# Performance work log

Hardware: AMD Instinct MI355X
Metric: run time of the kernel (lower is better)

## Reference

```python
import jax, jax.numpy as jnp
import numpy as np


def gru_layer(x, w_ih, w_hh, b_ih, b_hh):
    """PyTorch-semantics single GRU layer, batch_first.
    x: [B, T, in], w_ih: [3H, in], w_hh: [3H, H], gate order (r, z, n).
    Returns [B, T, H]. Initial hidden state is zeros.
    """
    H = w_hh.shape[1]
    # Precompute input-side gate projections for all timesteps (one big GEMM).
    xg = jnp.einsum('bti,gi->btg', x, w_ih) + b_ih  # [B, T, 3H]

    def step(h, xg_t):
        hg = h @ w_hh.T + b_hh                      # [B, 3H]
        xr, xz, xn = jnp.split(xg_t, 3, axis=-1)
        hr, hz, hn = jnp.split(hg, 3, axis=-1)
        r = jax.nn.sigmoid(xr + hr)
        z = jax.nn.sigmoid(xz + hz)
        n = jnp.tanh(xn + r * hn)
        h_new = (1.0 - z) * n + z * h
        return h_new, h_new

    h0 = jnp.zeros((x.shape[0], H), dtype=x.dtype)
    _, ys = jax.lax.scan(step, h0, jnp.swapaxes(xg, 0, 1))  # scan over T
    return jnp.swapaxes(ys, 0, 1)                           # [B, T, H]


def _make_layer(key, in_dim, hidden):
    k = 1.0 / np.sqrt(hidden)
    k1, k2, k3, k4 = jax.random.split(key, 4)
    w_ih = jax.random.uniform(k1, (3 * hidden, in_dim), jnp.float32, -k, k)
    w_hh = jax.random.uniform(k2, (3 * hidden, hidden), jnp.float32, -k, k)
    b_ih = jax.random.uniform(k3, (3 * hidden,), jnp.float32, -k, k)
    b_hh = jax.random.uniform(k4, (3 * hidden,), jnp.float32, -k, k)
    return w_ih, w_hh, b_ih, b_hh


def setup_inputs() -> dict:
    key = jax.random.key(0)
    B, C0, T = 32, 256, 2048
    H1, H2 = 512, 1024  # block0: 256->512 (2 layers), block1: 512->1024 (2 layers)
    keys = jax.random.split(key, 5)
    inp = {"x": jax.random.normal(keys[0], (B, C0, T), dtype=jnp.float32)}
    layer_dims = [(C0, H1), (H1, H1), (H1, H2), (H2, H2)]
    names = ['00', '01', '10', '11']
    for nm, (din, h), k in zip(names, layer_dims, keys[1:]):
        w_ih, w_hh, b_ih, b_hh = _make_layer(k, din, h)
        inp[f'w_ih_{nm}'] = w_ih
        inp[f'w_hh_{nm}'] = w_hh
        inp[f'b_ih_{nm}'] = b_ih
        inp[f'b_hh_{nm}'] = b_hh
    return inp


def reference(x,
              w_ih_00, w_hh_00, b_ih_00, b_hh_00,
              w_ih_01, w_hh_01, b_ih_01, b_hh_01,
              w_ih_10, w_hh_10, b_ih_10, b_hh_10,
              w_ih_11, w_hh_11, b_ih_11, b_hh_11):
    h = jnp.transpose(x, (0, 2, 1))  # [B, T, C]
    # Block 0 (2 stacked layers)
    h = gru_layer(h, w_ih_00, w_hh_00, b_ih_00, b_hh_00)
    h = gru_layer(h, w_ih_01, w_hh_01, b_ih_01, b_hh_01)
    # Block 1 (2 stacked layers)
    h = gru_layer(h, w_ih_10, w_hh_10, b_ih_10, b_hh_10)
    h = gru_layer(h, w_ih_11, w_hh_11, b_ih_11, b_hh_11)
    return jnp.transpose(h, (0, 2, 1))  # [B, H_last, T]
```

## Files before the change

### kernel.cpp

```cpp
#include <hip/hip_runtime.h>
#include <cstdint>
#include <cstddef>

typedef __attribute__((ext_vector_type(8))) __bf16 bhalf8;
typedef __attribute__((ext_vector_type(4))) float floatx4;

#define B_ 32
#define T_ 2048
#define CTR_STRIDE 32

__device__ __forceinline__ float sigm_f(float x){ return 1.0f / (1.0f + __expf(-x)); }
__device__ __forceinline__ float tanh_f(float x){ return 1.0f - 2.0f / (1.0f + __expf(2.0f*x)); }

__global__ void k_init(unsigned* bars){
  int i = blockIdx.x * 256 + threadIdx.x;
  if (i < 4 * 8 * CTR_STRIDE) bars[i] = 0u;
}

__global__ void k_cvt(const float* __restrict__ s, __bf16* __restrict__ d, int n){
  int i = blockIdx.x * 256 + threadIdx.x;
  if (i < n) d[i] = (__bf16)s[i];
}

template<typename TI, typename TO>
__global__ void k_transpose(const TI* __restrict__ in, TO* __restrict__ out, int R, int C){
  __shared__ float tile[32][33];
  const size_t bo = (size_t)blockIdx.z * (size_t)R * (size_t)C;
  const int c0 = blockIdx.x * 32, r0 = blockIdx.y * 32;
  const int tx = threadIdx.x, ty = threadIdx.y;
#pragma unroll
  for (int k2 = 0; k2 < 4; ++k2)
    tile[ty + k2*8][tx] = (float)in[bo + (size_t)(r0 + ty + k2*8) * C + c0 + tx];
  __syncthreads();
#pragma unroll
  for (int k2 = 0; k2 < 4; ++k2)
    out[bo + (size_t)(c0 + ty + k2*8) * R + r0 + tx] = (TO)tile[tx][ty + k2*8];
}

__global__ __launch_bounds__(256) void k_gemm(
    const __bf16* __restrict__ A, const __bf16* __restrict__ W,
    const float* __restrict__ bias, __bf16* __restrict__ C,
    int M, int N, int K)
{
  const int tid = threadIdx.x, wave = tid >> 6, lane = tid & 63;
  const int quad = lane >> 4, l = lane & 15;
  const int wy = wave >> 1, wx = wave & 1;
  const size_t rA = (size_t)blockIdx.y * 128 + (size_t)wy * 64;
  const size_t rW = (size_t)blockIdx.x * 128 + (size_t)wx * 64;
  floatx4 acc[4][4] = {};
  for (int k0 = 0; k0 < K; k0 += 32){
    bhalf8 af[4], wf[4];
#pragma unroll
    for (int i = 0; i < 4; ++i)
      af[i] = *(const bhalf8*)(A + (rA + 16*i + l) * (size_t)K + k0 + quad*8);
#pragma unroll
    for (int j = 0; j < 4; ++j)
      wf[j] = *(const bhalf8*)(W + (rW + 16*j + l) * (size_t)K + k0 + quad*8);
#pragma unroll
    for (int i = 0; i < 4; ++i)
#pragma unroll
      for (int j = 0; j < 4; ++j)
        acc[i][j] = __builtin_amdgcn_mfma_f32_16x16x32_bf16(af[i], wf[j], acc[i][j], 0, 0, 0);
  }
#pragma unroll
  for (int j = 0; j < 4; ++j){
    const float bv = bias[rW + 16*j + l];
#pragma unroll
    for (int i = 0; i < 4; ++i)
#pragma unroll
      for (int r = 0; r < 4; ++r)
        C[(rA + 16*i + quad*4 + r) * (size_t)N + rW + 16*j + l] = (__bf16)(acc[i][j][r] + bv);
  }
}

__device__ __forceinline__ void grid_barrier8(unsigned* bars, int my_ctr, unsigned per_target){
  __syncthreads();
  if (threadIdx.x < 8){
    if ((int)threadIdx.x == my_ctr)
      __hip_atomic_fetch_add(bars + my_ctr * CTR_STRIDE, 1u,
                             __ATOMIC_RELAXED, __HIP_MEMORY_SCOPE_AGENT);
    while (__hip_atomic_load(bars + threadIdx.x * CTR_STRIDE,
                             __ATOMIC_RELAXED, __HIP_MEMORY_SCOPE_AGENT) < per_target)
      __builtin_amdgcn_s_sleep(1);
  }
  __syncthreads();
}

__device__ __forceinline__ bhalf8 load_coherent16(const __bf16* p){
  union { unsigned long long q[2]; bhalf8 v; } u;
  u.q[0] = __hip_atomic_load((const unsigned long long*)p,     __ATOMIC_RELAXED, __HIP_MEMORY_SCOPE_AGENT);
  u.q[1] = __hip_atomic_load((const unsigned long long*)p + 1, __ATOMIC_RELAXED, __HIP_MEMORY_SCOPE_AGENT);
  return u.v;
}

template<int H>
__global__ __launch_bounds__(256) void k_scan(
    const __bf16* __restrict__ xg,
    const __bf16* __restrict__ whh,
    const float*  __restrict__ bhh,
    __bf16* __restrict__ hb0, __bf16* __restrict__ hb1,
    __bf16* __restrict__ Y,
    unsigned* __restrict__ bar)
{
  __shared__ float part[2*3*2*16*17];
  __shared__ float hown[32*17];
  const int tid = threadIdx.x, wave = tid >> 6, lane = tid & 63;
  const int quad = lane >> 4, l = lane & 15;
  const int m = wave & 1, kh = wave >> 1;
  const unsigned nblk = gridDim.x;
  const int bid = blockIdx.x;
  const int my_ctr = bid & 7;
  const int swz = (bid & 7) * ((int)nblk >> 3) + (bid >> 3);
  const int u0 = swz * 16;
  const unsigned per_blk = nblk >> 3;

  for (int i = tid; i < 32*16; i += 256){
    int b = i >> 4, u = i & 15;
    hown[b*17 + u] = 0.0f;
  }
  for (int i = tid; i < 32*8; i += 256){
    int b = i >> 3, d = i & 7;
    __hip_atomic_store((unsigned*)(hb0 + (size_t)b*H + u0) + d, 0u,
                       __ATOMIC_RELAXED, __HIP_MEMORY_SCOPE_AGENT);
  }
  const float bh0 = bhh[0*H + u0 + l];
  const float bh1 = bhh[1*H + u0 + l];
  const float bh2 = bhh[2*H + u0 + l];
  const __bf16* wr0 = whh + (size_t)(0*H + u0 + l)*H + kh*(H/2);
  const __bf16* wr1 = whh + (size_t)(1*H + u0 + l)*H + kh*(H/2);
  const __bf16* wr2 = whh + (size_t)(2*H + u0 + l)*H + kh*(H/2);
  const __bf16* ar0 = hb0 + (size_t)(16*m + l)*H + kh*(H/2);
  const __bf16* ar1 = hb1 + (size_t)(16*m + l)*H + kh*(H/2);
  const int b0g = 16*m + quad*4 + 2*kh;

  auto xgi = [&](int b, int t, int g)->size_t {
    return ((size_t)b*T_ + t)*(size_t)(3*H) + (size_t)g*H + u0 + l;
  };

  __bf16 xq[3][2];
#pragma unroll
  for (int g = 0; g < 3; ++g)
#pragma unroll
    for (int r2 = 0; r2 < 2; ++r2)
      xq[g][r2] = xg[xgi(b0g + r2, 0, g)];

  grid_barrier8(bar, my_ctr, per_blk);

  for (int t = 0; t < T_; ++t){
    const __bf16* ar = (t & 1) ? ar1 : ar0;
    __bf16* hd = (t & 1) ? hb0 : hb1;
    floatx4 a0 = {0.f,0.f,0.f,0.f}, a1 = a0, a2 = a0;
#pragma unroll
    for (int ks = 0; ks < H/64; ++ks){
      bhalf8 av = load_coherent16(ar + ks*32 + quad*8);
      bhalf8 w0 = *(const bhalf8*)(wr0 + ks*32 + quad*8);
      bhalf8 w1 = *(const bhalf8*)(wr1 + ks*32 + quad*8);
      bhalf8 w2 = *(const bhalf8*)(wr2 + ks*32 + quad*8);
      a0 = __builtin_amdgcn_mfma_f32_16x16x32_bf16(av, w0, a0, 0, 0, 0);
      a1 = __builtin_amdgcn_mfma_f32_16x16x32_bf16(av, w1, a1, 0, 0, 0);
      a2 = __builtin_amdgcn_mfma_f32_16x16x32_bf16(av, w2, a2, 0, 0, 0);
    }
    const int sb = (kh*6 + m)*272;
#pragma unroll
    for (int r = 0; r < 4; ++r){
      part[sb +        (quad*4+r)*17 + l] = a0[r];
      part[sb + 544  + (quad*4+r)*17 + l] = a1[r];
      part[sb + 1088 + (quad*4+r)*17 + l] = a2[r];
    }
    __syncthreads();
#pragma unroll
    for (int r2 = 0; r2 < 2; ++r2){
      const int row = quad*4 + 2*kh + r2;
      const int bb  = 16*m + row;
      const float hr = part[(0+m)*272 + row*17 + l] + part[(6+m)*272  + row*17 + l] + bh0;
      const float hz = part[(2+m)*272 + row*17 + l] + part[(8+m)*272  + row*17 + l] + bh1;
      const float hn = part[(4+m)*272 + row*17 + l] + part[(10+m)*272 + row*17 + l] + bh2;
      const float xr = (float)xq[0][r2], xz = (float)xq[1][r2], xn = (float)xq[2][r2];
      const float rg = sigm_f(xr + hr);
      const float zg = sigm_f(xz + hz);
      const float ng = tanh_f(xn + rg*hn);
      const float hp = hown[bb*17 + l];
      const float hnew = (1.0f - zg)*ng + zg*hp;
      hown[bb*17 + l] = hnew;
      const __bf16 hb16 = (__bf16)hnew;
      const unsigned mybits = (unsigned)__builtin_bit_cast(unsigned short, hb16);
      const unsigned other  = (unsigned)__shfl_xor((int)mybits, 1);
      if ((l & 1) == 0){
        const unsigned packed = mybits | (other << 16);
        __hip_atomic_store((unsigned*)(hd + (size_t)bb*H + u0 + l), packed,
                           __ATOMIC_RELAXED, __HIP_MEMORY_SCOPE_AGENT);
        __builtin_nontemporal_store(packed, (unsigned*)(Y + ((size_t)bb*T_ + t)*H + u0 + l));
      }
    }
    if (t + 1 < T_){
#pragma unroll
      for (int g = 0; g < 3; ++g)
#pragma unroll
        for (int r2 = 0; r2 < 2; ++r2)
          xq[g][r2] = xg[xgi(b0g + r2, t + 1, g)];
      grid_barrier8(bar, my_ctr, per_blk * (unsigned)(t + 2));
    }
  }
}

extern "C" void kernel_launch(void* const* d_in, const int* in_sizes, int n_in,
                              void* d_out, int out_size, void* d_ws, size_t ws_size,
                              hipStream_t stream) {
  (void)in_sizes; (void)n_in; (void)out_size; (void)ws_size;
  const float* x = (const float*)d_in[0];
  const float* wih[4] = {(const float*)d_in[1], (const float*)d_in[5], (const float*)d_in[9],  (const float*)d_in[13]};
  const float* whh[4] = {(const float*)d_in[2], (const float*)d_in[6], (const float*)d_in[10], (const float*)d_in[14]};
  const float* bih[4] = {(const float*)d_in[3], (const float*)d_in[7], (const float*)d_in[11], (const float*)d_in[15]};
  const float* bhh[4] = {(const float*)d_in[4], (const float*)d_in[8], (const float*)d_in[12], (const float*)d_in[16]};
  float* out = (float*)d_out;

  char* ws = (char*)d_ws;
  size_t off = 0;
  auto take = [&](size_t bytes)->char* {
    char* p = ws + off; off = (off + bytes + 255) & ~(size_t)255; return p;
  };
  const int IN[4] = {256, 512, 512, 1024};
  const int HH[4] = {512, 512, 1024, 1024};

  unsigned* bars = (unsigned*)take((size_t)4 * 8 * CTR_STRIDE * sizeof(unsigned));
  __bf16* wihb[4]; __bf16* whhb[4];
  for (int i = 0; i < 4; ++i){
    wihb[i] = (__bf16*)take((size_t)3*HH[i]*IN[i]*2);
    whhb[i] = (__bf16*)take((size_t)3*HH[i]*HH[i]*2);
  }
  __bf16* XG  = (__bf16*)take((size_t)B_*T_*3*1024*2);
  __bf16* Ya  = (__bf16*)take((size_t)B_*T_*1024*2);
  __bf16* Yb  = (__bf16*)take((size_t)B_*T_*1024*2);
  __bf16* hba = (__bf16*)take((size_t)B_*1024*2);
  __bf16* hbb = (__bf16*)take((size_t)B_*1024*2);
  __bf16* X0  = Yb;

  k_init<<<4, 256, 0, stream>>>(bars);
  for (int i = 0; i < 4; ++i){
    const int nih = 3*HH[i]*IN[i], nhh = 3*HH[i]*HH[i];
    k_cvt<<<(nih + 255)/256, 256, 0, stream>>>(wih[i], wihb[i], nih);
    k_cvt<<<(nhh + 255)/256, 256, 0, stream>>>(whh[i], whhb[i], nhh);
  }
  k_transpose<float, __bf16><<<dim3(T_/32, 256/32, B_), dim3(32, 8), 0, stream>>>(x, X0, 256, T_);

  const int M = B_ * T_;
  k_gemm<<<dim3(1536/128, M/128), 256, 0, stream>>>(X0, wihb[0], bih[0], XG, M, 1536, 256);
  k_scan<512><<<32, 256, 0, stream>>>(XG, whhb[0], bhh[0], hba, hbb, Ya, bars + 0*8*CTR_STRIDE);
  k_gemm<<<dim3(1536/128, M/128), 256, 0, stream>>>(Ya, wihb[1], bih[1], XG, M, 1536, 512);
  k_scan<512><<<32, 256, 0, stream>>>(XG, whhb[1], bhh[1], hba, hbb, Yb, bars + 1*8*CTR_STRIDE);
  k_gemm<<<dim3(3072/128, M/128), 256, 0, stream>>>(Yb, wihb[2], bih[2], XG, M, 3072, 512);
  k_scan<1024><<<64, 256, 0, stream>>>(XG, whhb[2], bhh[2], hba, hbb, Ya, bars + 2*8*CTR_STRIDE);
  k_gemm<<<dim3(3072/128, M/128), 256, 0, stream>>>(Ya, wihb[3], bih[3], XG, M, 3072, 1024);
  k_scan<1024><<<64, 256, 0, stream>>>(XG, whhb[3], bhh[3], hba, hbb, Yb, bars + 3*8*CTR_STRIDE);
  k_transpose<__bf16, float><<<dim3(1024/32, T_/32, B_), dim3(32, 8), 0, stream>>>(Yb, out, T_, 1024);
}
```

Measured before the change: 43.07 ms.

## Fuse all four GRU layers into one wavefront-pipelined persistent scan kernel

Replaces four sequential scan kernels and three input-projection GEMMs with a single persistent kernel of 192 blocks. Each layer's block group runs timestep t = s - L, so all layers advance together in T+3 grid-barrier steps. Layers 1-3 compute their input projection inside the recurrent step using packed [W_ih | W_hh] weights. This removes the large intermediate GEMMs, their XG traffic, and most of the serial barrier steps. In exchange, each step takes longer: layer-3 waves handle a K of 1024 instead of 512, and the barrier now spans every block. It also relies on all 192 blocks being resident at once.

Measured after the change: 40.72 ms. 5.5% less time.

```diff
diff --git a/kernel.cpp b/kernel.cpp
--- a/kernel.cpp
+++ b/kernel.cpp
@@ -8,18 +8,29 @@
 #define B_ 32
 #define T_ 2048
 #define CTR_STRIDE 32
+#define NCTR 16
+#define NBLK 192
 
 __device__ __forceinline__ float sigm_f(float x){ return 1.0f / (1.0f + __expf(-x)); }
 __device__ __forceinline__ float tanh_f(float x){ return 1.0f - 2.0f / (1.0f + __expf(2.0f*x)); }
 
 __global__ void k_init(unsigned* bars){
   int i = blockIdx.x * 256 + threadIdx.x;
-  if (i < 4 * 8 * CTR_STRIDE) bars[i] = 0u;
+  if (i < NCTR * CTR_STRIDE) bars[i] = 0u;
 }
 
 __global__ void k_cvt(const float* __restrict__ s, __bf16* __restrict__ d, int n){
   int i = blockIdx.x * 256 + threadIdx.x;
   if (i < n) d[i] = (__bf16)s[i];
+}
+
+__global__ void k_pack(const float* __restrict__ s, __bf16* __restrict__ d,
+                       int R, int C, int dstride, int doff){
+  int i = blockIdx.x * 256 + threadIdx.x;
+  if (i < R * C){
+    int r = i / C, c = i - r * C;
+    d[(size_t)r * dstride + doff + c] = (__bf16)s[i];
+  }
 }
 
 template<typename TI, typename TO>
@@ -73,15 +84,15 @@
   }
 }
 
-__device__ __forceinline__ void grid_barrier8(unsigned* bars, int my_ctr, unsigned per_target){
+__device__ __forceinline__ void grid_barrier16(unsigned* bars, int my_ctr, unsigned target){
   __syncthreads();
-  if (threadIdx.x < 8){
+  if (threadIdx.x < NCTR){
     if ((int)threadIdx.x == my_ctr)
       __hip_atomic_fetch_add(bars + my_ctr * CTR_STRIDE, 1u,
                              __ATOMIC_RELAXED, __HIP_MEMORY_SCOPE_AGENT);
     while (__hip_atomic_load(bars + threadIdx.x * CTR_STRIDE,
-                             __ATOMIC_RELAXED, __HIP_MEMORY_SCOPE_AGENT) < per_target)
-      __builtin_amdgcn_s_sleep(1);
+                             __ATOMIC_RELAXED, __HIP_MEMORY_SCOPE_AGENT) < target)
+      __builtin_amdgcn_s_sleep(2);
   }
   __syncthreads();
 }
@@ -93,114 +104,158 @@
   return u.v;
 }
 
-template<int H>
-__global__ __launch_bounds__(256) void k_scan(
-    const __bf16* __restrict__ xg,
-    const __bf16* __restrict__ whh,
-    const float*  __restrict__ bhh,
-    __bf16* __restrict__ hb0, __bf16* __restrict__ hb1,
-    __bf16* __restrict__ Y,
-    unsigned* __restrict__ bar)
+template<int LEN>
+__device__ __forceinline__ void gemm3(const __bf16* __restrict__ a,
+    const __bf16* __restrict__ w0, const __bf16* __restrict__ w1,
+    const __bf16* __restrict__ w2, int quad,
+    floatx4& a0, floatx4& a1, floatx4& a2)
+{
+#pragma unroll
+  for (int ks = 0; ks < LEN/32; ++ks){
+    bhalf8 av = load_coherent16(a + ks*32 + quad*8);
+    bhalf8 v0 = *(const bhalf8*)(w0 + ks*32 + quad*8);
+    bhalf8 v1 = *(const bhalf8*)(w1 + ks*32 + quad*8);
+    bhalf8 v2 = *(const bhalf8*)(w2 + ks*32 + quad*8);
+    a0 = __builtin_amdgcn_mfma_f32_16x16x32_bf16(av, v0, a0, 0, 0, 0);
+    a1 = __builtin_amdgcn_mfma_f32_16x16x32_bf16(av, v1, a1, 0, 0, 0);
+    a2 = __builtin_amdgcn_mfma_f32_16x16x32_bf16(av, v2, a2, 0, 0, 0);
+  }
+}
+
+struct ScanArgs {
+  const __bf16* xg0;
+  const __bf16* w[4];
+  const float*  bih[4];
+  const float*  bhh[4];
+  __bf16* h[4][2];
+  __bf16* Y;
+  unsigned* bar;
+};
+
+template<int L, int INDIM, int H>
+__device__ void run_layer(const ScanArgs& A, int lb, int nlb)
 {
   __shared__ float part[2*3*2*16*17];
   __shared__ float hown[32*17];
   const int tid = threadIdx.x, wave = tid >> 6, lane = tid & 63;
   const int quad = lane >> 4, l = lane & 15;
   const int m = wave & 1, kh = wave >> 1;
-  const unsigned nblk = gridDim.x;
-  const int bid = blockIdx.x;
-  const int my_ctr = bid & 7;
-  const int swz = (bid & 7) * ((int)nblk >> 3) + (bid >> 3);
+  const int swz = (lb & 7) * (nlb >> 3) + (lb >> 3);
   const int u0 = swz * 16;
-  const unsigned per_blk = nblk >> 3;
-
-  for (int i = tid; i < 32*16; i += 256){
-    int b = i >> 4, u = i & 15;
-    hown[b*17 + u] = 0.0f;
-  }
+  const int my_ctr = (int)(blockIdx.x & (NCTR - 1));
+  const unsigned per_ctr = NBLK / NCTR;
+
+  for (int i = tid; i < 32*16; i += 256){ int b = i >> 4, u = i & 15; hown[b*17 + u] = 0.0f; }
   for (int i = tid; i < 32*8; i += 256){
     int b = i >> 3, d = i & 7;
-    __hip_atomic_store((unsigned*)(hb0 + (size_t)b*H + u0) + d, 0u,
+    __hip_atomic_store((unsigned*)(A.h[L][0] + (size_t)b*H + u0) + d, 0u,
                        __ATOMIC_RELAXED, __HIP_MEMORY_SCOPE_AGENT);
   }
-  const float bh0 = bhh[0*H + u0 + l];
-  const float bh1 = bhh[1*H + u0 + l];
-  const float bh2 = bhh[2*H + u0 + l];
-  const __bf16* wr0 = whh + (size_t)(0*H + u0 + l)*H + kh*(H/2);
-  const __bf16* wr1 = whh + (size_t)(1*H + u0 + l)*H + kh*(H/2);
-  const __bf16* wr2 = whh + (size_t)(2*H + u0 + l)*H + kh*(H/2);
-  const __bf16* ar0 = hb0 + (size_t)(16*m + l)*H + kh*(H/2);
-  const __bf16* ar1 = hb1 + (size_t)(16*m + l)*H + kh*(H/2);
+  const float bb0 = A.bhh[L][0*H + u0 + l] + ((L > 0) ? A.bih[L][0*H + u0 + l] : 0.0f);
+  const float bb1 = A.bhh[L][1*H + u0 + l] + ((L > 0) ? A.bih[L][1*H + u0 + l] : 0.0f);
+  const float bxn = (L > 0) ? A.bih[L][2*H + u0 + l] : 0.0f;
+  const float bhn = A.bhh[L][2*H + u0 + l];
+
+  constexpr int WS = (L == 0) ? H : (INDIM + H);
+  const int wcb = (L == 0) ? kh*(H/2) : (kh ? INDIM : 0);
+  const __bf16* wp0 = A.w[L] + (size_t)(0*H + u0 + l)*WS + wcb;
+  const __bf16* wp1 = A.w[L] + (size_t)(1*H + u0 + l)*WS + wcb;
+  const __bf16* wp2 = A.w[L] + (size_t)(2*H + u0 + l)*WS + wcb;
+
+  const int arow = 16*m + l;
+  const __bf16* rec0 = A.h[L][0] + (size_t)arow*H + ((L == 0) ? kh*(H/2) : 0);
+  const __bf16* rec1 = A.h[L][1] + (size_t)arow*H + ((L == 0) ? kh*(H/2) : 0);
+  constexpr int LP = (L > 0) ? L - 1 : 0;
+  const __bf16* in0 = A.h[LP][0] + (size_t)arow*INDIM;
+  const __bf16* in1 = A.h[LP][1] + (size_t)arow*INDIM;
+
   const int b0g = 16*m + quad*4 + 2*kh;
 
-  auto xgi = [&](int b, int t, int g)->size_t {
-    return ((size_t)b*T_ + t)*(size_t)(3*H) + (size_t)g*H + u0 + l;
-  };
-
   __bf16 xq[3][2];
-#pragma unroll
-  for (int g = 0; g < 3; ++g)
-#pragma unroll
-    for (int r2 = 0; r2 < 2; ++r2)
-      xq[g][r2] = xg[xgi(b0g + r2, 0, g)];
-
-  grid_barrier8(bar, my_ctr, per_blk);
-
-  for (int t = 0; t < T_; ++t){
-    const __bf16* ar = (t & 1) ? ar1 : ar0;
-    __bf16* hd = (t & 1) ? hb0 : hb1;
-    floatx4 a0 = {0.f,0.f,0.f,0.f}, a1 = a0, a2 = a0;
-#pragma unroll
-    for (int ks = 0; ks < H/64; ++ks){
-      bhalf8 av = load_coherent16(ar + ks*32 + quad*8);
-      bhalf8 w0 = *(const bhalf8*)(wr0 + ks*32 + quad*8);
-      bhalf8 w1 = *(const bhalf8*)(wr1 + ks*32 + quad*8);
-      bhalf8 w2 = *(const bhalf8*)(wr2 + ks*32 + quad*8);
-      a0 = __builtin_amdgcn_mfma_f32_16x16x32_bf16(av, w0, a0, 0, 0, 0);
-      a1 = __builtin_amdgcn_mfma_f32_16x16x32_bf16(av, w1, a1, 0, 0, 0);
-      a2 = __builtin_amdgcn_mfma_f32_16x16x32_bf16(av, w2, a2, 0, 0, 0);
-    }
-    const int sb = (kh*6 + m)*272;
-#pragma unroll
-    for (int r = 0; r < 4; ++r){
-      part[sb +        (quad*4+r)*17 + l] = a0[r];
-      part[sb + 544  + (quad*4+r)*17 + l] = a1[r];
-      part[sb + 1088 + (quad*4+r)*17 + l] = a2[r];
-    }
-    __syncthreads();
-#pragma unroll
-    for (int r2 = 0; r2 < 2; ++r2){
-      const int row = quad*4 + 2*kh + r2;
-      const int bb  = 16*m + row;
-      const float hr = part[(0+m)*272 + row*17 + l] + part[(6+m)*272  + row*17 + l] + bh0;
-      const float hz = part[(2+m)*272 + row*17 + l] + part[(8+m)*272  + row*17 + l] + bh1;
-      const float hn = part[(4+m)*272 + row*17 + l] + part[(10+m)*272 + row*17 + l] + bh2;
-      const float xr = (float)xq[0][r2], xz = (float)xq[1][r2], xn = (float)xq[2][r2];
-      const float rg = sigm_f(xr + hr);
-      const float zg = sigm_f(xz + hz);
-      const float ng = tanh_f(xn + rg*hn);
-      const float hp = hown[bb*17 + l];
-      const float hnew = (1.0f - zg)*ng + zg*hp;
-      hown[bb*17 + l] = hnew;
-      const __bf16 hb16 = (__bf16)hnew;
-      const unsigned mybits = (unsigned)__builtin_bit_cast(unsigned short, hb16);
-      const unsigned other  = (unsigned)__shfl_xor((int)mybits, 1);
-      if ((l & 1) == 0){
-        const unsigned packed = mybits | (other << 16);
-        __hip_atomic_store((unsigned*)(hd + (size_t)bb*H + u0 + l), packed,
-                           __ATOMIC_RELAXED, __HIP_MEMORY_SCOPE_AGENT);
-        __builtin_nontemporal_store(packed, (unsigned*)(Y + ((size_t)bb*T_ + t)*H + u0 + l));
+  if constexpr (L == 0){
+#pragma unroll
+    for (int g = 0; g < 3; ++g)
+#pragma unroll
+      for (int r2 = 0; r2 < 2; ++r2)
+        xq[g][r2] = A.xg0[((size_t)(b0g + r2)*T_ + 0)*(size_t)(3*H) + (size_t)g*H + u0 + l];
+  }
+
+  grid_barrier16(A.bar, my_ctr, per_ctr * 1u);
+
+  for (int s = 0; s < T_ + 3; ++s){
+    const int t = s - L;
+    if (0 <= t && t < T_){
+      const int pr = t & 1;
+      floatx4 a0 = {0.f,0.f,0.f,0.f}, a1 = a0, a2 = a0;
+      if constexpr (L == 0){
+        gemm3<H/2>(pr ? rec1 : rec0, wp0, wp1, wp2, quad, a0, a1, a2);
+      } else {
+        if (kh == 0) gemm3<INDIM>(pr ? in0 : in1, wp0, wp1, wp2, quad, a0, a1, a2);
+        else         gemm3<H>(pr ? rec1 : rec0, wp0, wp1, wp2, quad, a0, a1, a2);
+      }
+      const int sb = (kh*6 + m)*272;
+#pragma unroll
+      for (int r = 0; r < 4; ++r){
+        part[sb +        (quad*4+r)*17 + l] = a0[r];
+        part[sb + 544  + (quad*4+r)*17 + l] = a1[r];
+        part[sb + 1088 + (quad*4+r)*17 + l] = a2[r];
+      }
+      __syncthreads();
+#pragma unroll
+      for (int r2 = 0; r2 < 2; ++r2){
+        const int row = quad*4 + 2*kh + r2;
+        const int bb  = 16*m + row;
+        const float pr_a = part[(0+m)*272 + row*17 + l], pr_b = part[(6+m)*272  + row*17 + l];
+        const float pz_a = part[(2+m)*272 + row*17 + l], pz_b = part[(8+m)*272  + row*17 + l];
+        const float pn_a = part[(4+m)*272 + row*17 + l], pn_b = part[(10+m)*272 + row*17 + l];
+        float rg, zg, ng;
+        if constexpr (L == 0){
+          const float xr = (float)xq[0][r2], xz = (float)xq[1][r2], xn = (float)xq[2][r2];
+          rg = sigm_f(xr + pr_a + pr_b + bb0);
+          zg = sigm_f(xz + pz_a + pz_b + bb1);
+          ng = tanh_f(xn + rg*(pn_a + pn_b + bhn));
+        } else {
+          rg = sigm_f(pr_a + pr_b + bb0);
+          zg = sigm_f(pz_a + pz_b + bb1);
+          ng = tanh_f(pn_a + bxn + rg*(pn_b + bhn));
+        }
+        const float hp = hown[bb*17 + l];
+        const float hnew = (1.0f - zg)*ng + zg*hp;
+        hown[bb*17 + l] = hnew;
+        const __bf16 hb16 = (__bf16)hnew;
+        const unsigned mybits = (unsigned)__builtin_bit_cast(unsigned short, hb16);
+        const unsigned other  = (unsigned)__shfl_xor((int)mybits, 1);
+        if ((l & 1) == 0){
+          const unsigned packed = mybits | (other << 16);
+          __bf16* hd = pr ? A.h[L][0] : A.h[L][1];
+          __hip_atomic_store((unsigned*)(hd + (size_t)bb*H + u0 + l), packed,
+                             __ATOMIC_RELAXED, __HIP_MEMORY_SCOPE_AGENT);
+          if constexpr (L == 3)
+            __builtin_nontemporal_store(packed, (unsigned*)(A.Y + ((size_t)bb*T_ + t)*H + u0 + l));
+        }
+      }
+      if constexpr (L == 0){
+        if (t + 1 < T_){
+#pragma unroll
+          for (int g = 0; g < 3; ++g)
+#pragma unroll
+            for (int r2 = 0; r2 < 2; ++r2)
+              xq[g][r2] = A.xg0[((size_t)(b0g + r2)*T_ + (t+1))*(size_t)(3*H) + (size_t)g*H + u0 + l];
+        }
       }
     }
-    if (t + 1 < T_){
-#pragma unroll
-      for (int g = 0; g < 3; ++g)
-#pragma unroll
-        for (int r2 = 0; r2 < 2; ++r2)
-          xq[g][r2] = xg[xgi(b0g + r2, t + 1, g)];
-      grid_barrier8(bar, my_ctr, per_blk * (unsigned)(t + 2));
-    }
-  }
+    if (s + 1 < T_ + 3)
+      grid_barrier16(A.bar, my_ctr, per_ctr * (unsigned)(s + 2));
+  }
+}
+
+__global__ __launch_bounds__(256) void k_scan4(ScanArgs A)
+{
+  const int bid = blockIdx.x;
+  if      (bid < 32)  run_layer<0,    0,  512>(A, bid,       32);
+  else if (bid < 64)  run_layer<1,  512,  512>(A, bid - 32,  32);
+  else if (bid < 128) run_layer<2,  512, 1024>(A, bid - 64,  64);
+  else                run_layer<3, 1024, 1024>(A, bid - 128, 64);
 }
 
 extern "C" void kernel_launch(void* const* d_in, const int* in_sizes, int n_in,
@@ -219,38 +274,44 @@
   auto take = [&](size_t bytes)->char* {
     char* p = ws + off; off = (off + bytes + 255) & ~(size_t)255; return p;
   };
-  const int IN[4] = {256, 512, 512, 1024};
+
+  unsigned* bars = (unsigned*)take((size_t)NCTR * CTR_STRIDE * sizeof(unsigned));
+  __bf16* wihb0 = (__bf16*)take((size_t)1536 *  256 * 2);
+  __bf16* whhb0 = (__bf16*)take((size_t)1536 *  512 * 2);
+  __bf16* WC1   = (__bf16*)take((size_t)1536 * 1024 * 2);
+  __bf16* WC2   = (__bf16*)take((size_t)3072 * 1536 * 2);
+  __bf16* WC3   = (__bf16*)take((size_t)3072 * 2048 * 2);
+  __bf16* XG0   = (__bf16*)take((size_t)B_*T_*1536*2);
+  __bf16* Yb    = (__bf16*)take((size_t)B_*T_*1024*2);
+  __bf16* hbuf[4][2];
   const int HH[4] = {512, 512, 1024, 1024};
-
-  unsigned* bars = (unsigned*)take((size_t)4 * 8 * CTR_STRIDE * sizeof(unsigned));
-  __bf16* wihb[4]; __bf16* whhb[4];
-  for (int i = 0; i < 4; ++i){
-    wihb[i] = (__bf16*)take((size_t)3*HH[i]*IN[i]*2);
-    whhb[i] = (__bf16*)take((size_t)3*HH[i]*HH[i]*2);
-  }
-  __bf16* XG  = (__bf16*)take((size_t)B_*T_*3*1024*2);
-  __bf16* Ya  = (__bf16*)take((size_t)B_*T_*1024*2);
-  __bf16* Yb  = (__bf16*)take((size_t)B_*T_*1024*2);
-  __bf16* hba = (__bf16*)take((size_t)B_*1024*2);
-  __bf16* hbb = (__bf16*)take((size_t)B_*1024*2);
-  __bf16* X0  = Yb;
-
-  k_init<<<4, 256, 0, stream>>>(bars);
-  for (int i = 0; i < 4; ++i){
-    const int nih = 3*HH[i]*IN[i], nhh = 3*HH[i]*HH[i];
-    k_cvt<<<(nih + 255)/256, 256, 0, stream>>>(wih[i], wihb[i], nih);
-    k_cvt<<<(nhh + 255)/256, 256, 0, stream>>>(whh[i], whhb[i], nhh);
-  }
+  for (int i = 0; i < 4; ++i)
+    for (int p = 0; p < 2; ++p)
+      hbuf[i][p] = (__bf16*)take((size_t)B_ * HH[i] * 2);
+  __bf16* X0 = Yb;
+
+  k_init<<<2, 256, 0, stream>>>(bars);
+  { const int n = 1536*256; k_cvt<<<(n+255)/256, 256, 0, stream>>>(wih[0], wihb0, n); }
+  { const int n = 1536*512; k_cvt<<<(n+255)/256, 256, 0, stream>>>(whh[0], whhb0, n); }
+  { int n=1536*512;  k_pack<<<(n+255)/256,256,0,stream>>>(wih[1], WC1, 1536,  512, 1024,    0); }
+  { int n=1536*512;  k_pack<<<(n+255)/256,256,0,stream>>>(whh[1], WC1, 1536,  512, 1024,  512); }
+  { int n=3072*512;  k_pack<<<(n+255)/256,256,0,stream>>>(wih[2], WC2, 3072,  512, 1536,    0); }
+  { int n=3072*1024; k_pack<<<(n+255)/256,256,0,stream>>>(whh[2], WC2, 3072, 1024, 1536,  512); }
+  { int n=3072*1024; k_pack<<<(n+255)/256,256,0,stream>>>(wih[3], WC3, 3072, 1024, 2048,    0); }
+  { int n=3072*1024; k_pack<<<(n+255)/256,256,0,stream>>>(whh[3], WC3, 3072, 1024, 2048, 1024); }
+
   k_transpose<float, __bf16><<<dim3(T_/32, 256/32, B_), dim3(32, 8), 0, stream>>>(x, X0, 256, T_);
 
   const int M = B_ * T_;
-  k_gemm<<<dim3(1536/128, M/128), 256, 0, stream>>>(X0, wihb[0], bih[0], XG, M, 1536, 256);
-  k_scan<512><<<32, 256, 0, stream>>>(XG, whhb[0], bhh[0], hba, hbb, Ya, bars + 0*8*CTR_STRIDE);
-  k_gemm<<<dim3(1536/128, M/128), 256, 0, stream>>>(Ya, wihb[1], bih[1], XG, M, 1536, 512);
-  k_scan<512><<<32, 256, 0, stream>>>(XG, whhb[1], bhh[1], hba, hbb, Yb, bars + 1*8*CTR_STRIDE);
-  k_gemm<<<dim3(3072/128, M/128), 256, 0, stream>>>(Yb, wihb[2], bih[2], XG, M, 3072, 512);
-  k_scan<1024><<<64, 256, 0, stream>>>(XG, whhb[2], bhh[2], hba, hbb, Ya, bars + 2*8*CTR_STRIDE);
-  k_gemm<<<dim3(3072/128, M/128), 256, 0, stream>>>(Ya, wihb[3], bih[3], XG, M, 3072, 1024);
-  k_scan<1024><<<64, 256, 0, stream>>>(XG, whhb[3], bhh[3], hba, hbb, Yb, bars + 3*8*CTR_STRIDE);
+  k_gemm<<<dim3(1536/128, M/128), 256, 0, stream>>>(X0, wihb0, bih[0], XG0, M, 1536, 256);
+
+  ScanArgs A;
+  A.xg0 = XG0;
+  A.w[0] = whhb0; A.w[1] = WC1; A.w[2] = WC2; A.w[3] = WC3;
+  for (int i = 0; i < 4; ++i){ A.bih[i] = bih[i]; A.bhh[i] = bhh[i]; }
+  for (int i = 0; i < 4; ++i) for (int p = 0; p < 2; ++p) A.h[i][p] = hbuf[i][p];
+  A.Y = Yb; A.bar = bars;
+  k_scan4<<<NBLK, 256, 0, stream>>>(A);
+
   k_transpose<__bf16, float><<<dim3(1024/32, T_/32, B_), dim3(32, 8), 0, stream>>>(Yb, out, T_, 1024);
 }
```
